# Kernel optimization log

Hardware: AMD Instinct MI355X
Metric: run time of the kernel (lower is better)

## Reference

```python
import jax, jax.numpy as jnp
import numpy as np

NUM_HEAD = 8   # in_channels // 64 for in_channels=512
DIM = 8        # per-head dim (== num_head in this module)
H_CH = NUM_HEAD * DIM  # 64
SCALE = DIM ** (-0.5)


def _conv(x, w, b, padding):
    # x: [N,C,H,W], w: [O,I,kh,kw]
    out = jax.lax.conv_general_dilated(
        x, w, window_strides=(1, 1), padding=padding,
        dimension_numbers=("NCHW", "OIHW", "NCHW"))
    return out + b[None, :, None, None]


def setup_inputs() -> dict:
    key = jax.random.key(0)
    ks = jax.random.split(key, 4)
    N, C, H, W = 4, 512, 48, 48
    x = jax.random.normal(ks[0], (N, C, H, W), dtype=jnp.float32)
    qkv_w = jax.random.normal(ks[1], (3 * H_CH, C, 1, 1), dtype=jnp.float32) * 0.05
    qkv_b = jnp.zeros((3 * H_CH,), dtype=jnp.float32)
    pos_w = jax.random.normal(ks[2], (H_CH, H_CH, 3, 3), dtype=jnp.float32) * 0.05
    pos_b = jnp.zeros((H_CH,), dtype=jnp.float32)
    res_w = jax.random.normal(ks[3], (C, H_CH, 1, 1), dtype=jnp.float32) * 0.05
    res_b = jnp.zeros((C,), dtype=jnp.float32)
    return {"x": x, "qkv_w": qkv_w, "qkv_b": qkv_b,
            "pos_w": pos_w, "pos_b": pos_b,
            "res_w": res_w, "res_b": res_b}


def reference(x, qkv_w, qkv_b, pos_w, pos_b, res_w, res_b):
    N, C, H, W = x.shape
    L = H * W
    # 1x1 conv QKV projection -> [N, 3h, H, W]
    qkv = _conv(x, qkv_w, qkv_b, "VALID")
    # [N, num_head, 3*dim, L]
    qkv = qkv.reshape(N, NUM_HEAD, 3 * DIM, L)
    q, k, v = qkv[:, :, :DIM], qkv[:, :, DIM:2 * DIM], qkv[:, :, 2 * DIM:]
    # attn = q^T @ k * scale : [N, nh, L, L], softmax over keys (last dim)
    attn = jnp.einsum("nhdq,nhdk->nhqk", q, k) * SCALE
    attn = jax.nn.softmax(attn, axis=-1)
    # out = v @ attn^T : [N, nh, dim, L]
    out = jnp.einsum("nhdk,nhqk->nhdq", v, attn)
    out = out.reshape(N, H_CH, H, W)
    # positional branch: 3x3 conv on v
    pos = _conv(v.reshape(N, H_CH, H, W), pos_w, pos_b, "SAME")
    out = out + pos
    # resume 1x1 conv -> [N, out_channels, H, W]
    return _conv(out, res_w, res_b, "VALID")
```

## Files before the change

### kernel.cpp

```cpp
#include <hip/hip_runtime.h>

#define L_ATT 2304
#define QSCALE_LOG2E 0.5100695712f

using bh8 = __attribute__((ext_vector_type(8))) short;
using f4  = __attribute__((ext_vector_type(4))) float;

#if __has_builtin(__builtin_amdgcn_exp2f)
#define EXP2(x) __builtin_amdgcn_exp2f(x)
#else
#define EXP2(x) exp2f(x)
#endif

__device__ inline short f2b(float f) {
    union { float f; unsigned u; } c; c.f = f;
    unsigned r = (c.u + 0x7FFFu + ((c.u >> 16) & 1u)) >> 16;
    return (short)r;
}
__device__ inline int packhi(float lo, float hi) {
    return (int)__builtin_amdgcn_perm(__float_as_uint(hi), __float_as_uint(lo), 0x07060302u);
}

__global__ __launch_bounds__(256) void wcvt_kernel(
    const float* __restrict__ qkv_w, const float* __restrict__ res_w,
    const float* __restrict__ pos_w,
    short* __restrict__ wqb, short* __restrict__ reswb, short* __restrict__ wqp)
{
    int j = blockIdx.x * 256 + threadIdx.x;
    if (j < 24576) {
        float4 v = ((const float4*)qkv_w)[j];
        short4 o = { f2b(v.x), f2b(v.y), f2b(v.z), f2b(v.w) };
        *(short4*)(wqb + (size_t)j * 4) = o;
    } else if (j < 32768) {
        int idx = j - 24576;
        float4 v = ((const float4*)res_w)[idx];
        short4 o = { f2b(v.x), f2b(v.y), f2b(v.z), f2b(v.w) };
        *(short4*)(reswb + (size_t)idx * 4) = o;
    } else if (j < 69632) {
        int e = j - 32768;
        wqp[e] = f2b(pos_w[(size_t)(e & 4095) * 9 + (e >> 12)]);
    }
}

__global__ __launch_bounds__(256) void xt_kernel(
    const float* __restrict__ x, short* __restrict__ xt)
{
    const int l0 = blockIdx.x * 64, k0 = blockIdx.y * 64, n = blockIdx.z;
    __shared__ float s[64][68];
    const int tr = threadIdx.x >> 4, tc4 = (threadIdx.x & 15) * 4;
    const float* xp = x + ((size_t)n * 512 + k0) * L_ATT + l0;
#pragma unroll
    for (int r = 0; r < 4; ++r)
        *(float4*)&s[tr + r * 16][tc4] =
            *(const float4*)(xp + (size_t)(tr + r * 16) * L_ATT + tc4);
    __syncthreads();
    short* op = xt + ((size_t)n * L_ATT + l0) * 512 + k0;
#pragma unroll
    for (int r = 0; r < 4; ++r) {
        int l = tr + r * 16;
        short4 o = { f2b(s[tc4 + 0][l]), f2b(s[tc4 + 1][l]),
                     f2b(s[tc4 + 2][l]), f2b(s[tc4 + 3][l]) };
        *(short4*)(op + (size_t)l * 512 + tc4) = o;
    }
}

__global__ __launch_bounds__(256) void qkv_kernel(
    const short* __restrict__ xt, const short* __restrict__ wqb,
    const float* __restrict__ qkv_b, short* __restrict__ qt8,
    short* __restrict__ kt8, short* __restrict__ vt, short* __restrict__ vle)
{
    const int g = blockIdx.x;
    const int xcd = g & 7, rr = g >> 3;
    const int y = rr % 3, grp = rr / 3;
    const int code = grp * 8 + xcd;
    const int l0 = (code % 36) * 64, oc0 = y * 64, n = code / 36;

    const int lane = threadIdx.x & 63, wave = threadIdx.x >> 6;
    const int col = lane & 15, quad = lane >> 4;
    const int ocb = oc0 + wave * 16;

    f4 acc[4];
#pragma unroll
    for (int nt = 0; nt < 4; ++nt) acc[nt] = (f4){0.f, 0.f, 0.f, 0.f};

    const short* arow = wqb + (size_t)(ocb + col) * 512 + quad * 8;
    const short* brow = xt + ((size_t)n * L_ATT + l0 + col) * 512 + quad * 8;

#pragma unroll 4
    for (int k0 = 0; k0 < 512; k0 += 32) {
        bh8 af = *(const bh8*)(arow + k0);
        bh8 b0 = *(const bh8*)(brow + k0);
        bh8 b1 = *(const bh8*)(brow + (size_t)16 * 512 + k0);
        bh8 b2 = *(const bh8*)(brow + (size_t)32 * 512 + k0);
        bh8 b3 = *(const bh8*)(brow + (size_t)48 * 512 + k0);
        acc[0] = __builtin_amdgcn_mfma_f32_16x16x32_bf16(af, b0, acc[0], 0, 0, 0);
        acc[1] = __builtin_amdgcn_mfma_f32_16x16x32_bf16(af, b1, acc[1], 0, 0, 0);
        acc[2] = __builtin_amdgcn_mfma_f32_16x16x32_bf16(af, b2, acc[2], 0, 0, 0);
        acc[3] = __builtin_amdgcn_mfma_f32_16x16x32_bf16(af, b3, acc[3], 0, 0, 0);
    }

    const int obase = ocb + quad * 4;
    const int h = obase / 24;
    const int r0 = obase - h * 24;
    const int slice = n * 8 + h;

#pragma unroll
    for (int nt = 0; nt < 4; ++nt) {
        int l = l0 + nt * 16 + col;
        float v[4];
#pragma unroll
        for (int reg = 0; reg < 4; ++reg) v[reg] = acc[nt][reg] + qkv_b[obase + reg];
        if (r0 < 8) {
            short4 o = { f2b(v[0] * QSCALE_LOG2E), f2b(v[1] * QSCALE_LOG2E),
                         f2b(v[2] * QSCALE_LOG2E), f2b(v[3] * QSCALE_LOG2E) };
            *(short4*)(qt8 + ((size_t)slice * L_ATT + l) * 8 + r0) = o;
        } else if (r0 < 16) {
            short4 o = { f2b(v[0]), f2b(v[1]), f2b(v[2]), f2b(v[3]) };
            *(short4*)(kt8 + ((size_t)slice * L_ATT + l) * 8 + (r0 - 8)) = o;
        } else {
            short4 o = { f2b(v[0]), f2b(v[1]), f2b(v[2]), f2b(v[3]) };
            int d0 = r0 - 16;
#pragma unroll
            for (int reg = 0; reg < 4; ++reg)
                vt[((size_t)slice * 8 + d0 + reg) * L_ATT + l] = ((short*)&o)[reg];
            *(short4*)(vle + ((size_t)n * L_ATT + l) * 64 + h * 8 + d0) = o;
        }
    }
}

__global__ __launch_bounds__(256) void attn_kernel(
    const short* __restrict__ qt8, const short* __restrict__ kt8,
    const short* __restrict__ vt, float* __restrict__ t32)
{
    const int g = blockIdx.x;
    const int h = g & 7, r = g >> 3;
    const int n = r / 18;
    const int q0 = (r % 18) * 128;
    const int slice = n * 8 + h;
    const int tid = threadIdx.x;
    const int lane = tid & 63, wave = tid >> 6;
    const int col = lane & 15, quad = lane >> 4;

    __shared__ short smem[2064];

    const short* qs  = qt8 + (size_t)slice * L_ATT * 8;
    const short* ks8 = kt8 + (size_t)slice * L_ATT * 8;
    const short* vb  = vt  + (size_t)slice * 8 * L_ATT;

    if (tid < 16) smem[2048 + tid] = (tid < 8) ? (short)0x3F80 : (short)0;

    bh8 zero8 = {0, 0, 0, 0, 0, 0, 0, 0};
    bh8 qf[2];
#pragma unroll
    for (int f = 0; f < 2; ++f) {
        qf[f] = zero8;
        if (quad == 0)
            qf[f] = *(const bh8*)(qs + (size_t)(q0 + wave * 32 + f * 16 + col) * 8);
    }

    const int kxor = (quad == 0) ? 512 : 0;
    int kidx[4];
#pragma unroll
    for (int nt = 0; nt < 4; ++nt)
        kidx[nt] = (quad == 0) ? (nt * 16 + col) * 8 : 2056;
    const int vxor = (col < 8) ? 512 : 0;
    int vidx[2];
#pragma unroll
    for (int ks = 0; ks < 2; ++ks)
        vidx[ks] = (col < 8)
                 ? 1024 + col * 64 + ((ks * 32 + quad * 8 + col * 8) & 63)
                 : ((col == 8) ? 2048 : 2056);

    const int ksl = ((lane >> 5) & 1) * 32 + ((lane >> 2) & 1) * 16
                  + ((lane >> 3) & 3) * 4 + (lane & 3);
    const int vd = lane >> 3, vkc = (lane & 7) * 8;
    const int vsl = 1024 + vd * 64 + ((vkc + vd * 8) & 63);

    if (wave == 0)
        *(uint4*)&smem[ksl * 8] = *(const uint4*)(ks8 + (size_t)lane * 8);
    else if (wave == 1)
        *(uint4*)&smem[vsl] = *(const uint4*)(vb + (size_t)vd * L_ATT + vkc);
    __syncthreads();

    f4 oacc[2];
    oacc[0] = (f4){0.f, 0.f, 0.f, 0.f};
    oacc[1] = (f4){0.f, 0.f, 0.f, 0.f};

    int sofs = 512;
    for (int t = 0; t < 36; ++t) {
        uint4 dk, dv;
        if (wave == 0)
            dk = *(const uint4*)(ks8 + (size_t)((t + 1) * 64 + lane) * 8);
        else if (wave == 1)
            dv = *(const uint4*)(vb + (size_t)vd * L_ATT + (t + 1) * 64 + vkc);

        bh8 kf[4], vf[2];
#pragma unroll
        for (int nt = 0; nt < 4; ++nt) kf[nt] = *(const bh8*)&smem[kidx[nt]];
#pragma unroll
        for (int ks = 0; ks < 2; ++ks) vf[ks] = *(const bh8*)&smem[vidx[ks]];

#pragma unroll
        for (int f = 0; f < 2; ++f) {
            f4 s[4];
#pragma unroll
            for (int nt = 0; nt < 4; ++nt) {
                f4 z = (f4){0.f, 0.f, 0.f, 0.f};
                s[nt] = __builtin_amdgcn_mfma_f32_16x16x32_bf16(kf[nt], qf[f], z, 0, 0, 0);
            }
            float e[4][4];
#pragma unroll
            for (int nt = 0; nt < 4; ++nt)
#pragma unroll
                for (int reg = 0; reg < 4; ++reg)
                    e[nt][reg] = EXP2(s[nt][reg]);
#pragma unroll
            for (int ks = 0; ks < 2; ++ks) {
                union { int i[4]; bh8 v; } pu;
                pu.i[0] = packhi(e[2 * ks][0],     e[2 * ks][1]);
                pu.i[1] = packhi(e[2 * ks][2],     e[2 * ks][3]);
                pu.i[2] = packhi(e[2 * ks + 1][0], e[2 * ks + 1][1]);
                pu.i[3] = packhi(e[2 * ks + 1][2], e[2 * ks + 1][3]);
                oacc[f] = __builtin_amdgcn_mfma_f32_16x16x32_bf16(vf[ks], pu.v, oacc[f], 0, 0, 0);
            }
        }

        if (wave == 0)      *(uint4*)&smem[sofs + ksl * 8] = dk;
        else if (wave == 1) *(uint4*)&smem[sofs + vsl] = dv;

#pragma unroll
        for (int nt = 0; nt < 4; ++nt) kidx[nt] ^= kxor;
        vidx[0] ^= vxor; vidx[1] ^= vxor;
        sofs ^= 512;
        __syncthreads();
    }

#pragma unroll
    for (int f = 0; f < 2; ++f) {
        float ls = __shfl(oacc[f][0], 32 + col, 64);
        float inv = 1.0f / ls;
        if (quad < 2) {
            int qg = q0 + wave * 32 + f * 16 + col;
            float4 o = { oacc[f][0] * inv, oacc[f][1] * inv,
                         oacc[f][2] * inv, oacc[f][3] * inv };
            *(float4*)(t32 + ((size_t)n * L_ATT + qg) * 64 + h * 8 + quad * 4) = o;
        }
    }
}

__global__ __launch_bounds__(256) void posconv_kernel(
    const short* __restrict__ vle, const short* __restrict__ wqp,
    const float* __restrict__ pbias, const float* __restrict__ t32,
    short* __restrict__ tbh)
{
    const int n = blockIdx.y;
    const int lane = threadIdx.x & 63;
    const int t = threadIdx.x >> 6;
    const int l0 = blockIdx.x * 16;
    const int col = lane & 15, quad = lane >> 4;

    const int la = l0 + col;
    const int ya = la / 48, xa = la - ya * 48;

    f4 acc = (f4){0.f, 0.f, 0.f, 0.f};
    const short* vbase = vle + (size_t)n * L_ATT * 64;

#pragma unroll
    for (int q = 0; q < 9; ++q) {
        const int dy = q / 3 - 1, dx = q - (q / 3) * 3 - 1;
        const bool valid = ((unsigned)(ya + dy) < 48u) && ((unsigned)(xa + dx) < 48u);
        const short* ap = vbase + (size_t)(la + dy * 48 + dx) * 64 + quad * 8;
#pragma unroll
        for (int ks = 0; ks < 2; ++ks) {
            bh8 af = {0, 0, 0, 0, 0, 0, 0, 0};
            if (valid) af = *(const bh8*)(ap + ks * 32);
            bh8 bf = *(const bh8*)(wqp + ((size_t)q * 64 + t * 16 + col) * 64
                                   + ks * 32 + quad * 8);
            acc = __builtin_amdgcn_mfma_f32_16x16x32_bf16(af, bf, acc, 0, 0, 0);
        }
    }

    const float* tp = t32 + (size_t)n * L_ATT * 64;
    short* op = tbh + (size_t)n * L_ATT * 64;
    const int oc = t * 16 + col;
    const float bb = pbias[oc];
#pragma unroll
    for (int reg = 0; reg < 4; ++reg) {
        int l = l0 + quad * 4 + reg;
        size_t idx = (size_t)l * 64 + oc;
        op[idx] = f2b(acc[reg] + tp[idx] + bb);
    }
}

__global__ __launch_bounds__(256) void res_kernel(
    const short* __restrict__ tbh, const short* __restrict__ reswb,
    const float* __restrict__ res_b, float* __restrict__ out)
{
    const int g = blockIdx.x;
    const int xcd = g & 7, rr = g >> 3;
    const int y = rr & 7, grp = rr >> 3;
    const int code = grp * 8 + xcd;
    const int l0 = (code % 36) * 64, oc0 = y * 64, n = code / 36;

    const int lane = threadIdx.x & 63, wave = threadIdx.x >> 6;
    const int col = lane & 15, quad = lane >> 4;
    const int ocb = oc0 + wave * 16;

    f4 acc[4];
#pragma unroll
    for (int nt = 0; nt < 4; ++nt) acc[nt] = (f4){0.f, 0.f, 0.f, 0.f};

#pragma unroll
    for (int ks = 0; ks < 2; ++ks) {
        bh8 af = *(const bh8*)(reswb + (size_t)(ocb + col) * 64 + ks * 32 + quad * 8);
#pragma unroll
        for (int nt = 0; nt < 4; ++nt) {
            bh8 bf = *(const bh8*)(tbh + ((size_t)n * L_ATT + l0 + nt * 16 + col) * 64
                                   + ks * 32 + quad * 8);
            acc[nt] = __builtin_amdgcn_mfma_f32_16x16x32_bf16(af, bf, acc[nt], 0, 0, 0);
        }
    }

#pragma unroll
    for (int nt = 0; nt < 4; ++nt) {
        int l = l0 + nt * 16 + col;
#pragma unroll
        for (int reg = 0; reg < 4; ++reg) {
            int oc = ocb + quad * 4 + reg;
            out[((size_t)n * 512 + oc) * L_ATT + l] = acc[nt][reg] + res_b[oc];
        }
    }
}

extern "C" void kernel_launch(void* const* d_in, const int* in_sizes, int n_in,
                              void* d_out, int out_size, void* d_ws, size_t ws_size,
                              hipStream_t stream)
{
    const float* x      = (const float*)d_in[0];
    const float* qkv_w  = (const float*)d_in[1];
    const float* qkv_b  = (const float*)d_in[2];
    const float* pos_w  = (const float*)d_in[3];
    const float* pos_b  = (const float*)d_in[4];
    const float* res_w  = (const float*)d_in[5];
    const float* res_b  = (const float*)d_in[6];
    float* out = (float*)d_out;

    char* ws = (char*)d_ws;
    short* xt    = (short*)(ws);
    short* qt8   = (short*)(ws + 9437184);
    short* kt8   = (short*)(ws + 10616832);
    short* vt    = (short*)(ws + 11796480);
    short* tbh   = (short*)(ws + 12976128);
    short* wqb   = (short*)(ws + 14155776);
    short* reswb = (short*)(ws + 14352384);
    short* vle   = (short*)(ws + 14417920);
    short* wqp   = (short*)(ws + 15597568);
    float* t32   = (float*)d_out;

    wcvt_kernel<<<272, 256, 0, stream>>>(qkv_w, res_w, pos_w, wqb, reswb, wqp);
    xt_kernel<<<dim3(36, 8, 4), 256, 0, stream>>>(x, xt);
    qkv_kernel<<<432, 256, 0, stream>>>(xt, wqb, qkv_b, qt8, kt8, vt, vle);
    attn_kernel<<<576, 256, 0, stream>>>(qt8, kt8, vt, t32);
    posconv_kernel<<<dim3(144, 4), 256, 0, stream>>>(vle, wqp, pos_b, t32, tbh);
    res_kernel<<<1152, 256, 0, stream>>>(tbh, reswb, res_b, out);
}
```

Before: 163.3 us.

## Merge prep kernels and run posconv alongside attention in one launch

```diff
diff --git a/kernel.cpp b/kernel.cpp
--- a/kernel.cpp
+++ b/kernel.cpp
@@ -17,36 +17,42 @@
     unsigned r = (c.u + 0x7FFFu + ((c.u >> 16) & 1u)) >> 16;
     return (short)r;
 }
+__device__ inline float b2f(short s) {
+    union { unsigned u; float f; } c;
+    c.u = ((unsigned)(unsigned short)s) << 16;
+    return c.f;
+}
 __device__ inline int packhi(float lo, float hi) {
     return (int)__builtin_amdgcn_perm(__float_as_uint(hi), __float_as_uint(lo), 0x07060302u);
 }
 
-__global__ __launch_bounds__(256) void wcvt_kernel(
-    const float* __restrict__ qkv_w, const float* __restrict__ res_w,
-    const float* __restrict__ pos_w,
-    short* __restrict__ wqb, short* __restrict__ reswb, short* __restrict__ wqp)
-{
-    int j = blockIdx.x * 256 + threadIdx.x;
-    if (j < 24576) {
-        float4 v = ((const float4*)qkv_w)[j];
-        short4 o = { f2b(v.x), f2b(v.y), f2b(v.z), f2b(v.w) };
-        *(short4*)(wqb + (size_t)j * 4) = o;
-    } else if (j < 32768) {
-        int idx = j - 24576;
-        float4 v = ((const float4*)res_w)[idx];
-        short4 o = { f2b(v.x), f2b(v.y), f2b(v.z), f2b(v.w) };
-        *(short4*)(reswb + (size_t)idx * 4) = o;
-    } else if (j < 69632) {
-        int e = j - 32768;
-        wqp[e] = f2b(pos_w[(size_t)(e & 4095) * 9 + (e >> 12)]);
-    }
-}
-
-__global__ __launch_bounds__(256) void xt_kernel(
-    const float* __restrict__ x, short* __restrict__ xt)
-{
-    const int l0 = blockIdx.x * 64, k0 = blockIdx.y * 64, n = blockIdx.z;
+__global__ __launch_bounds__(256) void prep_kernel(
+    const float* __restrict__ x, const float* __restrict__ qkv_w,
+    const float* __restrict__ res_w, const float* __restrict__ pos_w,
+    short* __restrict__ xt, short* __restrict__ wqb,
+    short* __restrict__ reswb, short* __restrict__ wqp)
+{
     __shared__ float s[64][68];
+    const int g = blockIdx.x;
+    if (g < 272) {
+        int j = g * 256 + threadIdx.x;
+        if (j < 24576) {
+            float4 v = ((const float4*)qkv_w)[j];
+            short4 o = { f2b(v.x), f2b(v.y), f2b(v.z), f2b(v.w) };
+            *(short4*)(wqb + (size_t)j * 4) = o;
+        } else if (j < 32768) {
+            int idx = j - 24576;
+            float4 v = ((const float4*)res_w)[idx];
+            short4 o = { f2b(v.x), f2b(v.y), f2b(v.z), f2b(v.w) };
+            *(short4*)(reswb + (size_t)idx * 4) = o;
+        } else {
+            int e = j - 32768;
+            wqp[e] = f2b(pos_w[(size_t)(e & 4095) * 9 + (e >> 12)]);
+        }
+        return;
+    }
+    const int gg = g - 272;
+    const int l0 = (gg % 36) * 64, k0 = ((gg / 36) & 7) * 64, n = gg / 288;
     const int tr = threadIdx.x >> 4, tc4 = (threadIdx.x & 15) * 4;
     const float* xp = x + ((size_t)n * 512 + k0) * L_ATT + l0;
 #pragma unroll
@@ -128,136 +134,133 @@
     }
 }
 
-__global__ __launch_bounds__(256) void attn_kernel(
+__global__ __launch_bounds__(256) void attnpos_kernel(
     const short* __restrict__ qt8, const short* __restrict__ kt8,
-    const short* __restrict__ vt, float* __restrict__ t32)
-{
+    const short* __restrict__ vt, const short* __restrict__ vle,
+    const short* __restrict__ wqp, const float* __restrict__ pbias,
+    float* __restrict__ t32, short* __restrict__ pcv)
+{
+    __shared__ short smem[2064];
     const int g = blockIdx.x;
-    const int h = g & 7, r = g >> 3;
-    const int n = r / 18;
-    const int q0 = (r % 18) * 128;
-    const int slice = n * 8 + h;
     const int tid = threadIdx.x;
     const int lane = tid & 63, wave = tid >> 6;
     const int col = lane & 15, quad = lane >> 4;
 
-    __shared__ short smem[2064];
-
-    const short* qs  = qt8 + (size_t)slice * L_ATT * 8;
-    const short* ks8 = kt8 + (size_t)slice * L_ATT * 8;
-    const short* vb  = vt  + (size_t)slice * 8 * L_ATT;
-
-    if (tid < 16) smem[2048 + tid] = (tid < 8) ? (short)0x3F80 : (short)0;
-
-    bh8 zero8 = {0, 0, 0, 0, 0, 0, 0, 0};
-    bh8 qf[2];
-#pragma unroll
-    for (int f = 0; f < 2; ++f) {
-        qf[f] = zero8;
-        if (quad == 0)
-            qf[f] = *(const bh8*)(qs + (size_t)(q0 + wave * 32 + f * 16 + col) * 8);
-    }
-
-    const int kxor = (quad == 0) ? 512 : 0;
-    int kidx[4];
-#pragma unroll
-    for (int nt = 0; nt < 4; ++nt)
-        kidx[nt] = (quad == 0) ? (nt * 16 + col) * 8 : 2056;
-    const int vxor = (col < 8) ? 512 : 0;
-    int vidx[2];
-#pragma unroll
-    for (int ks = 0; ks < 2; ++ks)
-        vidx[ks] = (col < 8)
-                 ? 1024 + col * 64 + ((ks * 32 + quad * 8 + col * 8) & 63)
-                 : ((col == 8) ? 2048 : 2056);
-
-    const int ksl = ((lane >> 5) & 1) * 32 + ((lane >> 2) & 1) * 16
-                  + ((lane >> 3) & 3) * 4 + (lane & 3);
-    const int vd = lane >> 3, vkc = (lane & 7) * 8;
-    const int vsl = 1024 + vd * 64 + ((vkc + vd * 8) & 63);
-
-    if (wave == 0)
-        *(uint4*)&smem[ksl * 8] = *(const uint4*)(ks8 + (size_t)lane * 8);
-    else if (wave == 1)
-        *(uint4*)&smem[vsl] = *(const uint4*)(vb + (size_t)vd * L_ATT + vkc);
-    __syncthreads();
-
-    f4 oacc[2];
-    oacc[0] = (f4){0.f, 0.f, 0.f, 0.f};
-    oacc[1] = (f4){0.f, 0.f, 0.f, 0.f};
-
-    int sofs = 512;
-    for (int t = 0; t < 36; ++t) {
-        uint4 dk, dv;
+    if (g < 576) {
+        const int h = g & 7, r = g >> 3;
+        const int n = r / 18;
+        const int q0 = (r % 18) * 128;
+        const int slice = n * 8 + h;
+
+        const short* qs  = qt8 + (size_t)slice * L_ATT * 8;
+        const short* ks8 = kt8 + (size_t)slice * L_ATT * 8;
+        const short* vb  = vt  + (size_t)slice * 8 * L_ATT;
+
+        if (tid < 16) smem[2048 + tid] = (tid < 8) ? (short)0x3F80 : (short)0;
+
+        bh8 zero8 = {0, 0, 0, 0, 0, 0, 0, 0};
+        bh8 qf[2];
+#pragma unroll
+        for (int f = 0; f < 2; ++f) {
+            qf[f] = zero8;
+            if (quad == 0)
+                qf[f] = *(const bh8*)(qs + (size_t)(q0 + wave * 32 + f * 16 + col) * 8);
+        }
+
+        const int kxor = (quad == 0) ? 512 : 0;
+        int kidx[4];
+#pragma unroll
+        for (int nt = 0; nt < 4; ++nt)
+            kidx[nt] = (quad == 0) ? (nt * 16 + col) * 8 : 2056;
+        const int vxor = (col < 8) ? 512 : 0;
+        int vidx[2];
+#pragma unroll
+        for (int ks = 0; ks < 2; ++ks)
+            vidx[ks] = (col < 8)
+                     ? 1024 + col * 64 + ((ks * 32 + quad * 8 + col * 8) & 63)
+                     : ((col == 8) ? 2048 : 2056);
+
+        const int ksl = ((lane >> 5) & 1) * 32 + ((lane >> 2) & 1) * 16
+                      + ((lane >> 3) & 3) * 4 + (lane & 3);
+        const int vd = lane >> 3, vkc = (lane & 7) * 8;
+        const int vsl = 1024 + vd * 64 + ((vkc + vd * 8) & 63);
+
         if (wave == 0)
-            dk = *(const uint4*)(ks8 + (size_t)((t + 1) * 64 + lane) * 8);
+            *(uint4*)&smem[ksl * 8] = *(const uint4*)(ks8 + (size_t)lane * 8);
         else if (wave == 1)
-            dv = *(const uint4*)(vb + (size_t)vd * L_ATT + (t + 1) * 64 + vkc);
-
-        bh8 kf[4], vf[2];
-#pragma unroll
-        for (int nt = 0; nt < 4; ++nt) kf[nt] = *(const bh8*)&smem[kidx[nt]];
-#pragma unroll
-        for (int ks = 0; ks < 2; ++ks) vf[ks] = *(const bh8*)&smem[vidx[ks]];
+            *(uint4*)&smem[vsl] = *(const uint4*)(vb + (size_t)vd * L_ATT + vkc);
+        __syncthreads();
+
+        f4 oacc[2];
+        oacc[0] = (f4){0.f, 0.f, 0.f, 0.f};
+        oacc[1] = (f4){0.f, 0.f, 0.f, 0.f};
+
+        int sofs = 512;
+        for (int t = 0; t < 36; ++t) {
+            uint4 dk, dv;
+            if (wave == 0)
+                dk = *(const uint4*)(ks8 + (size_t)((t + 1) * 64 + lane) * 8);
+            else if (wave == 1)
+                dv = *(const uint4*)(vb + (size_t)vd * L_ATT + (t + 1) * 64 + vkc);
+
+            bh8 kf[4], vf[2];
+#pragma unroll
+            for (int nt = 0; nt < 4; ++nt) kf[nt] = *(const bh8*)&smem[kidx[nt]];
+#pragma unroll
+            for (int ks = 0; ks < 2; ++ks) vf[ks] = *(const bh8*)&smem[vidx[ks]];
+
+#pragma unroll
+            for (int f = 0; f < 2; ++f) {
+                f4 s[4];
+#pragma unroll
+                for (int nt = 0; nt < 4; ++nt) {
+                    f4 z = (f4){0.f, 0.f, 0.f, 0.f};
+                    s[nt] = __builtin_amdgcn_mfma_f32_16x16x32_bf16(kf[nt], qf[f], z, 0, 0, 0);
+                }
+                float e[4][4];
+#pragma unroll
+                for (int nt = 0; nt < 4; ++nt)
+#pragma unroll
+                    for (int reg = 0; reg < 4; ++reg)
+                        e[nt][reg] = EXP2(s[nt][reg]);
+#pragma unroll
+                for (int ks = 0; ks < 2; ++ks) {
+                    union { int i[4]; bh8 v; } pu;
+                    pu.i[0] = packhi(e[2 * ks][0],     e[2 * ks][1]);
+                    pu.i[1] = packhi(e[2 * ks][2],     e[2 * ks][3]);
+                    pu.i[2] = packhi(e[2 * ks + 1][0], e[2 * ks + 1][1]);
+                    pu.i[3] = packhi(e[2 * ks + 1][2], e[2 * ks + 1][3]);
+                    oacc[f] = __builtin_amdgcn_mfma_f32_16x16x32_bf16(vf[ks], pu.v, oacc[f], 0, 0, 0);
+                }
+            }
+
+            if (wave == 0)      *(uint4*)&smem[sofs + ksl * 8] = dk;
+            else if (wave == 1) *(uint4*)&smem[sofs + vsl] = dv;
+
+#pragma unroll
+            for (int nt = 0; nt < 4; ++nt) kidx[nt] ^= kxor;
+            vidx[0] ^= vxor; vidx[1] ^= vxor;
+            sofs ^= 512;
+            __syncthreads();
+        }
 
 #pragma unroll
         for (int f = 0; f < 2; ++f) {
-            f4 s[4];
-#pragma unroll
-            for (int nt = 0; nt < 4; ++nt) {
-                f4 z = (f4){0.f, 0.f, 0.f, 0.f};
-                s[nt] = __builtin_amdgcn_mfma_f32_16x16x32_bf16(kf[nt], qf[f], z, 0, 0, 0);
+            float ls = __shfl(oacc[f][0], 32 + col, 64);
+            float inv = 1.0f / ls;
+            if (quad < 2) {
+                int qg = q0 + wave * 32 + f * 16 + col;
+                float4 o = { oacc[f][0] * inv, oacc[f][1] * inv,
+                             oacc[f][2] * inv, oacc[f][3] * inv };
+                *(float4*)(t32 + ((size_t)n * L_ATT + qg) * 64 + h * 8 + quad * 4) = o;
             }
-            float e[4][4];
-#pragma unroll
-            for (int nt = 0; nt < 4; ++nt)
-#pragma unroll
-                for (int reg = 0; reg < 4; ++reg)
-                    e[nt][reg] = EXP2(s[nt][reg]);
-#pragma unroll
-            for (int ks = 0; ks < 2; ++ks) {
-                union { int i[4]; bh8 v; } pu;
-                pu.i[0] = packhi(e[2 * ks][0],     e[2 * ks][1]);
-                pu.i[1] = packhi(e[2 * ks][2],     e[2 * ks][3]);
-                pu.i[2] = packhi(e[2 * ks + 1][0], e[2 * ks + 1][1]);
-                pu.i[3] = packhi(e[2 * ks + 1][2], e[2 * ks + 1][3]);
-                oacc[f] = __builtin_amdgcn_mfma_f32_16x16x32_bf16(vf[ks], pu.v, oacc[f], 0, 0, 0);
-            }
-        }
-
-        if (wave == 0)      *(uint4*)&smem[sofs + ksl * 8] = dk;
-        else if (wave == 1) *(uint4*)&smem[sofs + vsl] = dv;
-
-#pragma unroll
-        for (int nt = 0; nt < 4; ++nt) kidx[nt] ^= kxor;
-        vidx[0] ^= vxor; vidx[1] ^= vxor;
-        sofs ^= 512;
-        __syncthreads();
-    }
-
-#pragma unroll
-    for (int f = 0; f < 2; ++f) {
-        float ls = __shfl(oacc[f][0], 32 + col, 64);
-        float inv = 1.0f / ls;
-        if (quad < 2) {
-            int qg = q0 + wave * 32 + f * 16 + col;
-            float4 o = { oacc[f][0] * inv, oacc[f][1] * inv,
-                         oacc[f][2] * inv, oacc[f][3] * inv };
-            *(float4*)(t32 + ((size_t)n * L_ATT + qg) * 64 + h * 8 + quad * 4) = o;
-        }
-    }
-}
-
-__global__ __launch_bounds__(256) void posconv_kernel(
-    const short* __restrict__ vle, const short* __restrict__ wqp,
-    const float* __restrict__ pbias, const float* __restrict__ t32,
-    short* __restrict__ tbh)
-{
-    const int n = blockIdx.y;
-    const int lane = threadIdx.x & 63;
-    const int t = threadIdx.x >> 6;
-    const int l0 = blockIdx.x * 16;
-    const int col = lane & 15, quad = lane >> 4;
+        }
+        return;
+    }
+
+    const int gf = g - 576;
+    const int l0 = (gf % 144) * 16, n = gf / 144;
+    const int t = wave;
 
     const int la = l0 + col;
     const int ya = la / 48, xa = la - ya * 48;
@@ -280,21 +283,20 @@
         }
     }
 
-    const float* tp = t32 + (size_t)n * L_ATT * 64;
-    short* op = tbh + (size_t)n * L_ATT * 64;
+    short* op = pcv + (size_t)n * L_ATT * 64;
     const int oc = t * 16 + col;
     const float bb = pbias[oc];
 #pragma unroll
     for (int reg = 0; reg < 4; ++reg) {
         int l = l0 + quad * 4 + reg;
-        size_t idx = (size_t)l * 64 + oc;
-        op[idx] = f2b(acc[reg] + tp[idx] + bb);
+        op[(size_t)l * 64 + oc] = f2b(acc[reg] + bb);
     }
 }
 
 __global__ __launch_bounds__(256) void res_kernel(
-    const short* __restrict__ tbh, const short* __restrict__ reswb,
-    const float* __restrict__ res_b, float* __restrict__ out)
+    const float* __restrict__ t32, const short* __restrict__ pcv,
+    const short* __restrict__ reswb, const float* __restrict__ res_b,
+    float* __restrict__ out)
 {
     const int g = blockIdx.x;
     const int xcd = g & 7, rr = g >> 3;
@@ -315,9 +317,17 @@
         bh8 af = *(const bh8*)(reswb + (size_t)(ocb + col) * 64 + ks * 32 + quad * 8);
 #pragma unroll
         for (int nt = 0; nt < 4; ++nt) {
-            bh8 bf = *(const bh8*)(tbh + ((size_t)n * L_ATT + l0 + nt * 16 + col) * 64
-                                   + ks * 32 + quad * 8);
-            acc[nt] = __builtin_amdgcn_mfma_f32_16x16x32_bf16(af, bf, acc[nt], 0, 0, 0);
+            const size_t boff = ((size_t)n * L_ATT + l0 + nt * 16 + col) * 64
+                              + ks * 32 + quad * 8;
+            float4 ta = *(const float4*)(t32 + boff);
+            float4 tb = *(const float4*)(t32 + boff + 4);
+            bh8 pv = *(const bh8*)(pcv + boff);
+            union { int i[4]; bh8 v; } pu;
+            pu.i[0] = packhi(ta.x + b2f(pv[0]), ta.y + b2f(pv[1]));
+            pu.i[1] = packhi(ta.z + b2f(pv[2]), ta.w + b2f(pv[3]));
+            pu.i[2] = packhi(tb.x + b2f(pv[4]), tb.y + b2f(pv[5]));
+            pu.i[3] = packhi(tb.z + b2f(pv[6]), tb.w + b2f(pv[7]));
+            acc[nt] = __builtin_amdgcn_mfma_f32_16x16x32_bf16(af, pu.v, acc[nt], 0, 0, 0);
         }
     }
 
@@ -347,20 +357,18 @@
 
     char* ws = (char*)d_ws;
     short* xt    = (short*)(ws);
+    float* t32   = (float*)(ws);
     short* qt8   = (short*)(ws + 9437184);
     short* kt8   = (short*)(ws + 10616832);
     short* vt    = (short*)(ws + 11796480);
-    short* tbh   = (short*)(ws + 12976128);
+    short* pcv   = (short*)(ws + 12976128);
     short* wqb   = (short*)(ws + 14155776);
     short* reswb = (short*)(ws + 14352384);
     short* vle   = (short*)(ws + 14417920);
     short* wqp   = (short*)(ws + 15597568);
-    float* t32   = (float*)d_out;
-
-    wcvt_kernel<<<272, 256, 0, stream>>>(qkv_w, res_w, pos_w, wqb, reswb, wqp);
-    xt_kernel<<<dim3(36, 8, 4), 256, 0, stream>>>(x, xt);
+
+    prep_kernel<<<1424, 256, 0, stream>>>(x, qkv_w, res_w, pos_w, xt, wqb, reswb, wqp);
     qkv_kernel<<<432, 256, 0, stream>>>(xt, wqb, qkv_b, qt8, kt8, vt, vle);
-    attn_kernel<<<576, 256, 0, stream>>>(qt8, kt8, vt, t32);
-    posconv_kernel<<<dim3(144, 4), 256, 0, stream>>>(vle, wqp, pos_b, t32, tbh);
-    res_kernel<<<1152, 256, 0, stream>>>(tbh, reswb, res_b, out);
-}
+    attnpos_kernel<<<1152, 256, 0, stream>>>(qt8, kt8, vt, vle, wqp, pos_b, t32, pcv);
+    res_kernel<<<1152, 256, 0, stream>>>(t32, pcv, reswb, res_b, out);
+}
```

After: 158.5 us. -3.0%, faster.
